# Kernel tuning notes

Hardware: AMD Instinct MI355X
Metric: run time of the kernel (lower is better)

The kernel has to match this reference:

```python
import jax, jax.numpy as jnp
import numpy as np

# opt constants baked from init_kwargs
OPT_M = 1024      # number of OFDM subcarriers (opt.M)
N_PILOT = 0       # opt.N_pilot
VELOCITY = 100.0  # opt.V (is_random_v=False)
DECAY = 4.0       # opt.decay
C_LIGHT = 3.0e8
CARRIER_FREQ = 3.0e9


def setup_inputs() -> dict:
    key = jax.random.key(0)
    k1, k2 = jax.random.split(key, 2)
    N, P, L, M, S = 16, 4, 16, OPT_M, 128
    # channel tap power profile: exp(-l/decay), normalized
    power = jnp.exp(-jnp.arange(L, dtype=jnp.float32) / DECAY)
    power = power / jnp.sum(power)
    # Rayleigh(sigma=1) samples = sqrt(g1^2 + g2^2), g_i ~ N(0,1)
    g = jax.random.normal(k1, (N, P, L, 2), dtype=jnp.float32)
    rayleigh = jnp.sqrt(g[..., 0] ** 2 + g[..., 1] ** 2)
    cof = jnp.sqrt(power / 2.0) * rayleigh  # (N,P,L), strictly positive
    input_ri = jax.random.normal(k2, (N, P, S * M, 2), dtype=jnp.float32)
    return {"input_ri": input_ri, "cof": cof, "Ns": 128}


def reference(input_ri, cof, Ns):
    N, P, SMK, _ = input_ri.shape
    L = cof.shape[-1]
    S = Ns + N_PILOT  # OFDM mode: S = Ns + N_pilot, M = opt.M
    Mk = SMK // S
    x = (input_ri[..., 0] + 1j * input_ri[..., 1]).astype(jnp.complex64)  # (N,P,SMK)

    # per-tap propagation delay from tap gain: len = -100*log(cof); delay1 = len/c
    delay1 = (-100.0 * jnp.log(cof)) / C_LIGHT                      # (N,P,L)
    delay2 = jnp.linspace(0.0, (S - 1) * (0.0005 / 14.0), S).astype(jnp.float32)  # (S,)
    delay = delay1[..., None] + delay2                              # (N,P,L,S)

    max_doppler = VELOCITY / C_LIGHT * CARRIER_FREQ
    angles = jnp.linspace(0.0, 2.0 * np.pi, L).astype(jnp.float32)  # (L,)
    phase_coef = (2.0 * np.pi * jnp.cos(angles) * max_doppler)      # (L,)
    phases = phase_coef[None, None, :, None] * delay                # (N,P,L,S)
    shift = jnp.exp(-1j * phases.astype(jnp.float32))               # complex64 (N,P,L,S)

    # sum over taps L BEFORE multiplying by the L-independent input (same math,
    # avoids materializing the (N,P,L,S,M) broadcast intermediate)
    factor = jnp.sum(cof[..., None].astype(jnp.complex64) * shift, axis=2)  # (N,P,S)
    out = x.reshape(N, P, S, Mk) * factor[..., None]                # (N,P,S,M)
    out = out.reshape(N, P, SMK)
    out_ri = jnp.stack([out.real, out.imag], axis=-1)               # (N,P,SMK,2)

    # frequency response H_t = FFT of zero-padded taps
    cof_zp = jnp.concatenate([cof, jnp.zeros((N, P, OPT_M - L), cof.dtype)], axis=-1)
    H_t = jnp.fft.fft(cof_zp.astype(jnp.complex64), axis=-1)        # (N,P,OPT_M)
    H_t_ri = jnp.stack([H_t.real, H_t.imag], axis=-1)
    return out_ri, H_t_ri
```

## Files before the change

kernel.cpp:

```cpp
#include <hip/hip_runtime.h>
#include <math.h>

#define NB     16
#define PB     4
#define LTAPS  16
#define SS     128
#define MM     1024

__device__ __constant__ float C_LIGHT  = 3.0e8f;
#define TWO_PI_F 6.28318530717958647692f

__global__ __launch_bounds__(256) void main_kernel(
    const float* __restrict__ in,
    const float* __restrict__ cof,
    float* __restrict__ out)
{
    const int bid = blockIdx.x;
    const int np  = bid >> 7;
    const int s   = bid & (SS - 1);
    const int t   = threadIdx.x;

    __shared__ float lre[LTAPS], lim[LTAPS];

    if (t < LTAPS) {
        const float cofl   = cof[np * LTAPS + t];
        const float delay1 = (-100.0f * logf(cofl)) / C_LIGHT;
        const float delay2 = (0.0005f / 14.0f) * (float)s;
        const float angle  = (TWO_PI_F / 15.0f) * (float)t;
        const float pc     = TWO_PI_F * cosf(angle) * 1000.0f;
        const float ph     = pc * (delay1 + delay2);
        float sn, cs;
        sincosf(ph, &sn, &cs);
        lre[t] = cofl * cs;
        lim[t] = -cofl * sn;
    }
    __syncthreads();

    float fre = 0.0f, fim = 0.0f;
#pragma unroll
    for (int l = 0; l < LTAPS; ++l) { fre += lre[l]; fim += lim[l]; }

    const float4* __restrict__ in4  = (const float4*)in  + (size_t)bid * (MM / 2);
    float4* __restrict__       out4 = (float4*)out       + (size_t)bid * (MM / 2);

#pragma unroll
    for (int j = t; j < MM / 2; j += 256) {
        const float4 v = in4[j];
        float4 r;
        r.x = v.x * fre - v.y * fim;
        r.y = v.x * fim + v.y * fre;
        r.z = v.z * fre - v.w * fim;
        r.w = v.z * fim + v.w * fre;
        out4[j] = r;
    }
}

__global__ __launch_bounds__(256) void ht_kernel(
    const float* __restrict__ cof,
    float* __restrict__ ht)
{
    const int np = blockIdx.x;
    const int t  = threadIdx.x;

    __shared__ float c[LTAPS];
    if (t < LTAPS) c[t] = cof[np * LTAPS + t];
    __syncthreads();

    float2* __restrict__ o = (float2*)ht + (size_t)np * MM;

    for (int k = t; k < MM; k += 256) {
        float re = 0.0f, im = 0.0f;
#pragma unroll
        for (int l = 0; l < LTAPS; ++l) {
            const float ang = (TWO_PI_F / (float)MM) * (float)(k * l);
            float sn, cs;
            sincosf(ang, &sn, &cs);
            re += c[l] * cs;
            im -= c[l] * sn;
        }
        o[k] = make_float2(re, im);
    }
}

extern "C" void kernel_launch(void* const* d_in, const int* in_sizes, int n_in,
                              void* d_out, int out_size, void* d_ws, size_t ws_size,
                              hipStream_t stream)
{
    const float* in  = (const float*)d_in[0];
    const float* cof = (const float*)d_in[1];
    float* out = (float*)d_out;
    float* ht  = out + (size_t)NB * PB * SS * MM * 2;

    hipLaunchKernelGGL(main_kernel, dim3(NB * PB * SS), dim3(256), 0, stream,
                       in, cof, out);
    hipLaunchKernelGGL(ht_kernel, dim3(NB * PB), dim3(256), 0, stream,
                       cof, ht);
}
```

Before: 31.68 us.

## Precompute per-symbol factors in a small kernel and grid-stride the streaming multiply

Splits the work into a small kernel that computes all per-(n,p,s) complex factors into workspace and spreads the H_t DFT over 256 blocks, one output per thread. The main kernel becomes a grid-stride streaming complex multiply over 2048 blocks that reads those factors. This takes the shared-memory sync and serial tap reduction out of every streaming block, and it gives the H_t computation more parallelism. In exchange it adds a dependency between the two launches and an extra workspace round trip, and it drops the overlap of H_t with the main kernel.

```diff
diff --git a/kernel.cpp b/kernel.cpp
--- a/kernel.cpp
+++ b/kernel.cpp
@@ -7,78 +7,77 @@
 #define SS     128
 #define MM     1024
 
-__device__ __constant__ float C_LIGHT  = 3.0e8f;
 #define TWO_PI_F 6.28318530717958647692f
 
-__global__ __launch_bounds__(256) void main_kernel(
-    const float* __restrict__ in,
+#define FAC_BLKS  32
+#define HT_BLKS   256
+
+__global__ __launch_bounds__(256) void small_kernel(
     const float* __restrict__ cof,
-    float* __restrict__ out)
-{
-    const int bid = blockIdx.x;
-    const int np  = bid >> 7;
-    const int s   = bid & (SS - 1);
-    const int t   = threadIdx.x;
-
-    __shared__ float lre[LTAPS], lim[LTAPS];
-
-    if (t < LTAPS) {
-        const float cofl   = cof[np * LTAPS + t];
-        const float delay1 = (-100.0f * logf(cofl)) / C_LIGHT;
-        const float delay2 = (0.0005f / 14.0f) * (float)s;
-        const float angle  = (TWO_PI_F / 15.0f) * (float)t;
-        const float pc     = TWO_PI_F * cosf(angle) * 1000.0f;
-        const float ph     = pc * (delay1 + delay2);
-        float sn, cs;
-        sincosf(ph, &sn, &cs);
-        lre[t] = cofl * cs;
-        lim[t] = -cofl * sn;
-    }
-    __syncthreads();
-
-    float fre = 0.0f, fim = 0.0f;
-#pragma unroll
-    for (int l = 0; l < LTAPS; ++l) { fre += lre[l]; fim += lim[l]; }
-
-    const float4* __restrict__ in4  = (const float4*)in  + (size_t)bid * (MM / 2);
-    float4* __restrict__       out4 = (float4*)out       + (size_t)bid * (MM / 2);
-
-#pragma unroll
-    for (int j = t; j < MM / 2; j += 256) {
-        const float4 v = in4[j];
-        float4 r;
-        r.x = v.x * fre - v.y * fim;
-        r.y = v.x * fim + v.y * fre;
-        r.z = v.z * fre - v.w * fim;
-        r.w = v.z * fim + v.w * fre;
-        out4[j] = r;
-    }
-}
-
-__global__ __launch_bounds__(256) void ht_kernel(
-    const float* __restrict__ cof,
+    float* __restrict__ fac,
     float* __restrict__ ht)
 {
-    const int np = blockIdx.x;
-    const int t  = threadIdx.x;
+    const int b = blockIdx.x;
+    const int t = threadIdx.x;
 
-    __shared__ float c[LTAPS];
-    if (t < LTAPS) c[t] = cof[np * LTAPS + t];
-    __syncthreads();
-
-    float2* __restrict__ o = (float2*)ht + (size_t)np * MM;
-
-    for (int k = t; k < MM; k += 256) {
+    if (b < FAC_BLKS) {
+        const int id = b * 256 + t;
+        const int np = id >> 7;
+        const int s  = id & (SS - 1);
+        const float delay2 = (0.0005f / 14.0f) * (float)s;
+        float fre = 0.0f, fim = 0.0f;
+#pragma unroll
+        for (int l = 0; l < LTAPS; ++l) {
+            const float cofl   = cof[np * LTAPS + l];
+            const float delay1 = (-100.0f / 3.0e8f) * logf(cofl);
+            const float angle  = (TWO_PI_F / 15.0f) * (float)l;
+            const float pc     = TWO_PI_F * cosf(angle) * 1000.0f;
+            const float ph     = pc * (delay1 + delay2);
+            float sn, cs;
+            sincosf(ph, &sn, &cs);
+            fre += cofl * cs;
+            fim -= cofl * sn;
+        }
+        ((float2*)fac)[id] = make_float2(fre, fim);
+    } else {
+        const int id = (b - FAC_BLKS) * 256 + t;
+        const int np = id >> 10;
+        const int k  = id & (MM - 1);
         float re = 0.0f, im = 0.0f;
 #pragma unroll
         for (int l = 0; l < LTAPS; ++l) {
             const float ang = (TWO_PI_F / (float)MM) * (float)(k * l);
             float sn, cs;
             sincosf(ang, &sn, &cs);
-            re += c[l] * cs;
-            im -= c[l] * sn;
+            const float c = cof[np * LTAPS + l];
+            re += c * cs;
+            im -= c * sn;
         }
-        o[k] = make_float2(re, im);
+        ((float2*)ht)[id] = make_float2(re, im);
+    }
+}
+
+#define TOT4 (NB * PB * SS * MM / 2)
+
+__global__ __launch_bounds__(256) void main_kernel(
+    const float* __restrict__ in,
+    const float* __restrict__ fac,
+    float* __restrict__ out)
+{
+    const float2* __restrict__ f2 = (const float2*)fac;
+    const float4* __restrict__ in4 = (const float4*)in;
+    float4* __restrict__ out4 = (float4*)out;
+
+    const int stride = gridDim.x * 256;
+    for (int g = blockIdx.x * 256 + threadIdx.x; g < TOT4; g += stride) {
+        const float2 f = f2[g >> 9];
+        const float4 v = in4[g];
+        float4 r;
+        r.x = v.x * f.x - v.y * f.y;
+        r.y = v.x * f.y + v.y * f.x;
+        r.z = v.z * f.x - v.w * f.y;
+        r.w = v.z * f.y + v.w * f.x;
+        out4[g] = r;
     }
 }
 
@@ -90,9 +89,10 @@
     const float* cof = (const float*)d_in[1];
     float* out = (float*)d_out;
     float* ht  = out + (size_t)NB * PB * SS * MM * 2;
+    float* fac = (float*)d_ws;
 
-    hipLaunchKernelGGL(main_kernel, dim3(NB * PB * SS), dim3(256), 0, stream,
-                       in, cof, out);
-    hipLaunchKernelGGL(ht_kernel, dim3(NB * PB), dim3(256), 0, stream,
-                       cof, ht);
+    hipLaunchKernelGGL(small_kernel, dim3(FAC_BLKS + HT_BLKS), dim3(256), 0, stream,
+                       cof, fac, ht);
+    hipLaunchKernelGGL(main_kernel, dim3(2048), dim3(256), 0, stream,
+                       in, fac, out);
 }
```

Measured after the change: 30.86 us. -2.6%, faster.
